# Kernel tuning notes

Hardware: AMD Instinct MI355X
Metric: run time of the kernel (lower is better)

The kernel has to match this reference:

```python
import jax, jax.numpy as jnp
import numpy as np

D = 1024   # dim_mid
H = 16     # heads
DK = D // H  # d_k = d_v = 64
S = 2048   # seq_len
B = 1      # batch (module's reshape logic assumes batch==1)
EPS = 1e-5


def setup_inputs() -> dict:
    key = jax.random.key(0)
    ks = jax.random.split(key, 10)
    s = 0.02
    return dict(
        Q=jax.random.normal(ks[0], (B, S, D), dtype=jnp.float32),
        K=jax.random.normal(ks[1], (B, S, D), dtype=jnp.float32),
        V=jax.random.normal(ks[2], (B, S, D), dtype=jnp.float32),
        attn_mask=jax.random.randint(ks[3], (1, S, S), 0, 2).astype(bool),
        wq=jax.random.normal(ks[4], (H * DK, D), dtype=jnp.float32) * s,
        bq=jnp.zeros((H * DK,), dtype=jnp.float32),
        wk=jax.random.normal(ks[5], (H * DK, D), dtype=jnp.float32) * s,
        bk=jnp.zeros((H * DK,), dtype=jnp.float32),
        wv=jax.random.normal(ks[6], (H * DK, D), dtype=jnp.float32) * s,
        bv=jnp.zeros((H * DK,), dtype=jnp.float32),
        wo=jax.random.normal(ks[7], (D, H * DK), dtype=jnp.float32) * s,
        bo=jnp.zeros((D,), dtype=jnp.float32),
        gamma=jnp.ones((D,), dtype=jnp.float32),
        beta=jnp.zeros((D,), dtype=jnp.float32),
    )


def reference(Q, K, V, attn_mask, wq, bq, wk, bk, wv, bv, wo, bo, gamma, beta):
    b, s = Q.shape[0], Q.shape[1]
    # projections -> (B, H, S, d_k)
    q = (Q @ wq.T + bq).reshape(b, s, H, DK).transpose(0, 2, 1, 3)
    k = (K @ wk.T + bk).reshape(b, s, H, DK).transpose(0, 2, 1, 3)
    v = (V @ wv.T + bv).reshape(b, s, H, DK).transpose(0, 2, 1, 3)
    scores = jnp.einsum('bhqd,bhkd->bhqk', q, k) / np.float32(np.sqrt(DK))
    scores = jnp.where(attn_mask[:, None, :, :], jnp.float32(-1e9), scores)
    attn = jax.nn.softmax(scores, axis=-1)
    ctx = jnp.einsum('bhqk,bhkd->bhqd', attn, v)  # (B, H, S, d_v)
    # torch: squeeze(0).transpose(0,1).view(seq_len, -1, H*d_v)  (valid for B==1)
    ctx2 = ctx[0].transpose(1, 0, 2).reshape(s, 1, H * DK)  # (S, 1, H*d_v)
    out = (ctx2 @ wo.T + bo).transpose(1, 0, 2) + Q  # (1, S, D) residual
    mu = out.mean(-1, keepdims=True)
    var = out.var(-1, keepdims=True)
    out = (out - mu) / jnp.sqrt(var + EPS) * gamma + beta
    return out, attn, ctx2
```

## Files before the change

### kernel.cpp

```cpp
#include <hip/hip_runtime.h>
#include <stdint.h>

#define S_LEN 2048
#define D_MID 1024
#define N_HEADS 16
#define D_HEAD 64

typedef __attribute__((ext_vector_type(4))) float f32x4;
typedef __attribute__((ext_vector_type(8))) short bf16x8;

__device__ __forceinline__ unsigned short f2bf(float x) {
  unsigned int u = __builtin_bit_cast(unsigned int, x);
  u += 0x7fffu + ((u >> 16) & 1u);
  return (unsigned short)(u >> 16);
}
__device__ __forceinline__ float bf2f(unsigned short h) {
  unsigned int u = ((unsigned int)h) << 16;
  return __builtin_bit_cast(float, u);
}
__device__ __forceinline__ unsigned int pack2(float x, float y) {
  return (unsigned int)f2bf(x) | ((unsigned int)f2bf(y) << 16);
}

#define MFMA16(a, b, c) __builtin_amdgcn_mfma_f32_16x16x32_bf16((a), (b), (c), 0, 0, 0)

struct ProjParams {
  const float* A[3];
  const float* W[3];
  const float* B[3];
  unsigned short* O[3];
};

__global__ __launch_bounds__(256) void gemm_proj(ProjParams P) {
  const int z = blockIdx.z;
  const float* __restrict__ A = P.A[z];
  const float* __restrict__ W = P.W[z];
  const float* __restrict__ bias = P.B[z];
  unsigned short* __restrict__ O = P.O[z];

  __shared__ __align__(16) unsigned short As[128][56];
  __shared__ __align__(16) unsigned short Bs[128][56];

  const int tid = threadIdx.x;
  const int lane = tid & 63, w = tid >> 6;
  const int wm = w >> 1, wn = w & 1;
  const int l15 = lane & 15, lhi = lane >> 4;
  const int m0 = blockIdx.y * 128, n0 = blockIdx.x * 128;
  const int sr = tid >> 1, sc = (tid & 1) * 16;

  f32x4 acc[4][4] = {};

  for (int k0 = 0; k0 < D_MID; k0 += 32) {
    __syncthreads();
    {
      const float* a = A + (size_t)(m0 + sr) * D_MID + k0 + sc;
      float4 a0 = ((const float4*)a)[0], a1 = ((const float4*)a)[1];
      float4 a2 = ((const float4*)a)[2], a3 = ((const float4*)a)[3];
      uint4 wa0, wa1;
      wa0.x = pack2(a0.x, a0.y); wa0.y = pack2(a0.z, a0.w);
      wa0.z = pack2(a1.x, a1.y); wa0.w = pack2(a1.z, a1.w);
      wa1.x = pack2(a2.x, a2.y); wa1.y = pack2(a2.z, a2.w);
      wa1.z = pack2(a3.x, a3.y); wa1.w = pack2(a3.z, a3.w);
      *(uint4*)&As[sr][sc] = wa0;
      *(uint4*)&As[sr][sc + 8] = wa1;

      const float* b = W + (size_t)(n0 + sr) * D_MID + k0 + sc;
      float4 b0 = ((const float4*)b)[0], b1 = ((const float4*)b)[1];
      float4 b2 = ((const float4*)b)[2], b3 = ((const float4*)b)[3];
      uint4 wb0, wb1;
      wb0.x = pack2(b0.x, b0.y); wb0.y = pack2(b0.z, b0.w);
      wb0.z = pack2(b1.x, b1.y); wb0.w = pack2(b1.z, b1.w);
      wb1.x = pack2(b2.x, b2.y); wb1.y = pack2(b2.z, b2.w);
      wb1.z = pack2(b3.x, b3.y); wb1.w = pack2(b3.z, b3.w);
      *(uint4*)&Bs[sr][sc] = wb0;
      *(uint4*)&Bs[sr][sc + 8] = wb1;
    }
    __syncthreads();

    bf16x8 af[4], bfr[4];
#pragma unroll
    for (int a = 0; a < 4; ++a)
      af[a] = *(const bf16x8*)&As[wm * 64 + a * 16 + l15][lhi * 8];
#pragma unroll
    for (int b = 0; b < 4; ++b)
      bfr[b] = *(const bf16x8*)&Bs[wn * 64 + b * 16 + l15][lhi * 8];
#pragma unroll
    for (int a = 0; a < 4; ++a)
#pragma unroll
      for (int b = 0; b < 4; ++b) acc[a][b] = MFMA16(af[a], bfr[b], acc[a][b]);
  }

#pragma unroll
  for (int a = 0; a < 4; ++a)
#pragma unroll
    for (int b = 0; b < 4; ++b) {
      const int col = n0 + wn * 64 + b * 16 + l15;
      const float bv = bias[col];
#pragma unroll
      for (int j = 0; j < 4; ++j) {
        const int row = m0 + wm * 64 + a * 16 + lhi * 4 + j;
        O[(size_t)row * D_MID + col] = f2bf(acc[a][b][j] + bv);
      }
    }
}

__global__ __launch_bounds__(256) void gemm_out(
    const float* __restrict__ Actx, const float* __restrict__ W,
    const float* __restrict__ bias, const float* __restrict__ resid,
    float* __restrict__ Of) {
  __shared__ __align__(16) unsigned short As[128][56];
  __shared__ __align__(16) unsigned short Bs[128][56];

  const int tid = threadIdx.x;
  const int lane = tid & 63, w = tid >> 6;
  const int wm = w >> 1, wn = w & 1;
  const int l15 = lane & 15, lhi = lane >> 4;
  const int m0 = blockIdx.y * 128, n0 = blockIdx.x * 128;
  const int sr = tid >> 1, sc = (tid & 1) * 16;

  f32x4 acc[4][4] = {};

  for (int k0 = 0; k0 < D_MID; k0 += 32) {
    __syncthreads();
    {
      const float* a = Actx + (size_t)(m0 + sr) * D_MID + k0 + sc;
      float4 a0 = ((const float4*)a)[0], a1 = ((const float4*)a)[1];
      float4 a2 = ((const float4*)a)[2], a3 = ((const float4*)a)[3];
      uint4 wa0, wa1;
      wa0.x = pack2(a0.x, a0.y); wa0.y = pack2(a0.z, a0.w);
      wa0.z = pack2(a1.x, a1.y); wa0.w = pack2(a1.z, a1.w);
      wa1.x = pack2(a2.x, a2.y); wa1.y = pack2(a2.z, a2.w);
      wa1.z = pack2(a3.x, a3.y); wa1.w = pack2(a3.z, a3.w);
      *(uint4*)&As[sr][sc] = wa0;
      *(uint4*)&As[sr][sc + 8] = wa1;

      const float* b = W + (size_t)(n0 + sr) * D_MID + k0 + sc;
      float4 b0 = ((const float4*)b)[0], b1 = ((const float4*)b)[1];
      float4 b2 = ((const float4*)b)[2], b3 = ((const float4*)b)[3];
      uint4 wb0, wb1;
      wb0.x = pack2(b0.x, b0.y); wb0.y = pack2(b0.z, b0.w);
      wb0.z = pack2(b1.x, b1.y); wb0.w = pack2(b1.z, b1.w);
      wb1.x = pack2(b2.x, b2.y); wb1.y = pack2(b2.z, b2.w);
      wb1.z = pack2(b3.x, b3.y); wb1.w = pack2(b3.z, b3.w);
      *(uint4*)&Bs[sr][sc] = wb0;
      *(uint4*)&Bs[sr][sc + 8] = wb1;
    }
    __syncthreads();

    bf16x8 af[4], bfr[4];
#pragma unroll
    for (int a = 0; a < 4; ++a)
      af[a] = *(const bf16x8*)&As[wm * 64 + a * 16 + l15][lhi * 8];
#pragma unroll
    for (int b = 0; b < 4; ++b)
      bfr[b] = *(const bf16x8*)&Bs[wn * 64 + b * 16 + l15][lhi * 8];
#pragma unroll
    for (int a = 0; a < 4; ++a)
#pragma unroll
      for (int b = 0; b < 4; ++b) acc[a][b] = MFMA16(af[a], bfr[b], acc[a][b]);
  }

#pragma unroll
  for (int a = 0; a < 4; ++a)
#pragma unroll
    for (int b = 0; b < 4; ++b) {
      const int col = n0 + wn * 64 + b * 16 + l15;
      const float bv = bias[col];
#pragma unroll
      for (int j = 0; j < 4; ++j) {
        const int row = m0 + wm * 64 + a * 16 + lhi * 4 + j;
        Of[(size_t)row * D_MID + col] =
            acc[a][b][j] + bv + resid[(size_t)row * D_MID + col];
      }
    }
}

__global__ __launch_bounds__(256) void transpose_to_vbt(
    const unsigned short* __restrict__ v, unsigned short* __restrict__ vt) {
  __shared__ __align__(16) unsigned short t[64][72];
  const int tid = threadIdx.x;
  const int bs = blockIdx.x * 64;
  const int bd = blockIdx.y * 64;
  {
    const int r = tid >> 2, c = (tid & 3) * 16;
    const unsigned short* src = v + (size_t)(bs + r) * D_MID + bd + c;
    *(uint4*)&t[r][c] = *(const uint4*)src;
    *(uint4*)&t[r][c + 8] = *(const uint4*)(src + 8);
  }
  __syncthreads();
  {
    const int d = tid >> 2, c = (tid & 3) * 16;
    unsigned int u[8];
#pragma unroll
    for (int jj = 0; jj < 8; ++jj)
      u[jj] = (unsigned int)t[c + 2 * jj][d] | ((unsigned int)t[c + 2 * jj + 1][d] << 16);
    uint4 w0, w1;
    w0.x = u[0]; w0.y = u[1]; w0.z = u[2]; w0.w = u[3];
    w1.x = u[4]; w1.y = u[5]; w1.z = u[6]; w1.w = u[7];
    unsigned short* dst = vt + (size_t)(bd + d) * S_LEN + bs + c;
    *(uint4*)dst = w0;
    *(uint4*)(dst + 8) = w1;
  }
}

__global__ __launch_bounds__(256) void pack_mask(const void* __restrict__ maskp,
                                                 unsigned long long* __restrict__ bits) {
  __shared__ int s_m32;
  if (threadIdx.x == 0) s_m32 = 1;
  __syncthreads();
  {
    const unsigned char* m8d = (const unsigned char*)maskp;
    bool nz = false;
    for (int i = threadIdx.x; i < 4096; i += 256)
      if (i & 3) nz |= (m8d[i] != 0);
    if (nz) s_m32 = 0;
  }
  __syncthreads();

  const int wi = blockIdx.x * 256 + threadIdx.x;
  const int row = wi >> 5, chunk = wi & 31;
  unsigned long long keep = 0ull;
  if (s_m32) {
    const int* mi = (const int*)maskp + (size_t)row * S_LEN + chunk * 64;
#pragma unroll
    for (int q = 0; q < 16; ++q) {
      int4 v = ((const int4*)mi)[q];
      const int b = q * 4;
      if (!v.x) keep |= 1ull << b;
      if (!v.y) keep |= 1ull << (b + 1);
      if (!v.z) keep |= 1ull << (b + 2);
      if (!v.w) keep |= 1ull << (b + 3);
    }
  } else {
    const unsigned char* p = (const unsigned char*)maskp + (size_t)row * S_LEN + chunk * 64;
    union { uint4 v[4]; unsigned char c[64]; } u;
#pragma unroll
    for (int q = 0; q < 4; ++q) u.v[q] = ((const uint4*)p)[q];
#pragma unroll
    for (int b = 0; b < 64; ++b)
      if (!u.c[b]) keep |= 1ull << b;
  }
  bits[wi] = keep;
}

__global__ __launch_bounds__(256) void lsum_kernel(
    const unsigned short* __restrict__ qb, const unsigned short* __restrict__ kb,
    const unsigned long long* __restrict__ bits, float* __restrict__ lpart) {
  const int bid = blockIdx.x;
  const int head = bid & 15;
  const int r = bid >> 4;
  const int q0 = (r & 31) * 64;
  const int kc = r >> 5;
  const int k0 = kc * (S_LEN / 4);

  const int tid = threadIdx.x;
  const int lane = tid & 63, w = tid >> 6;
  const int l15 = lane & 15, lhi = lane >> 4;

  __shared__ __align__(16) unsigned short Kt[64][72];

  bf16x8 aq[2];
  {
    const unsigned short* qp =
        qb + (size_t)(q0 + w * 16 + l15) * D_MID + head * D_HEAD + lhi * 8;
    aq[0] = *(const bf16x8*)qp;
    aq[1] = *(const bf16x8*)(qp + 32);
  }

  float lrow[4] = {0.f, 0.f, 0.f, 0.f};
  const int sk = tid >> 2, sc = (tid & 3) * 16;

  for (int kt = k0; kt < k0 + S_LEN / 4; kt += 64) {
    __syncthreads();
    {
      const unsigned short* src = kb + (size_t)(kt + sk) * D_MID + head * D_HEAD + sc;
      *(uint4*)&Kt[sk][sc] = *(const uint4*)src;
      *(uint4*)&Kt[sk][sc + 8] = *(const uint4*)(src + 8);
    }
    __syncthreads();

    f32x4 sacc[4];
#pragma unroll
    for (int a = 0; a < 4; ++a) {
      bf16x8 b0 = *(const bf16x8*)&Kt[a * 16 + l15][lhi * 8];
      bf16x8 b1 = *(const bf16x8*)&Kt[a * 16 + l15][32 + lhi * 8];
      f32x4 t = {0.f, 0.f, 0.f, 0.f};
      t = MFMA16(aq[0], b0, t);
      t = MFMA16(aq[1], b1, t);
      sacc[a] = t;
    }

#pragma unroll
    for (int j = 0; j < 4; ++j) {
      const int qg = q0 + w * 16 + lhi * 4 + j;
      const unsigned long long w64 = bits[(size_t)qg * 32 + (kt >> 6)];
      float ts = 0.f;
#pragma unroll
      for (int a = 0; a < 4; ++a) {
        const float keep = (float)((w64 >> (a * 16 + l15)) & 1ull);
        ts += __expf(sacc[a][j] * 0.125f) * keep;
      }
#pragma unroll
      for (int off = 1; off < 16; off <<= 1) ts += __shfl_xor(ts, off);
      lrow[j] += ts;
    }
  }

  if (l15 == 0) {
#pragma unroll
    for (int j = 0; j < 4; ++j) {
      const int qg = q0 + w * 16 + lhi * 4 + j;
      lpart[((size_t)kc * N_HEADS + head) * S_LEN + qg] = lrow[j];
    }
  }
}

__global__ __launch_bounds__(256) void lcombine(const float* __restrict__ lpart,
                                                float* __restrict__ linv) {
  const int i = blockIdx.x * 256 + threadIdx.x;
  const float s = lpart[i] + lpart[32768 + i] + lpart[65536 + i] + lpart[98304 + i];
  linv[i] = (s > 0.f) ? 1.f / s : 0.f;
}

__global__ __launch_bounds__(256) void attn_main(
    const unsigned short* __restrict__ qb, const unsigned short* __restrict__ kb,
    const unsigned short* __restrict__ vbt, const unsigned long long* __restrict__ bits,
    const float* __restrict__ linv, float* __restrict__ attn_out,
    unsigned short* __restrict__ ctxp, int nkc) {
  const int bid = blockIdx.x;
  const int head = bid & 15;
  const int r = bid >> 4;
  const int q0 = (r & 31) * 64;
  const int kc = r >> 5;
  const int kspan = S_LEN / nkc;
  const int k_begin = kc * kspan;

  const int tid = threadIdx.x;
  const int lane = tid & 63, w = tid >> 6;
  const int l15 = lane & 15, lhi = lane >> 4;

  __shared__ __align__(16) unsigned short Kt[64][72];
  __shared__ __align__(16) unsigned short Vt[64][72];
  __shared__ __align__(16) unsigned short Pl[4][16][76];

  bf16x8 aq[2];
  float li[4];
  {
    const int qrow = q0 + w * 16 + l15;
    const unsigned short* qp = qb + (size_t)qrow * D_MID + head * D_HEAD + lhi * 8;
    aq[0] = *(const bf16x8*)qp;
    aq[1] = *(const bf16x8*)(qp + 32);
#pragma unroll
    for (int j = 0; j < 4; ++j)
      li[j] = linv[head * S_LEN + q0 + w * 16 + lhi * 4 + j];
  }

  f32x4 cacc[4] = {};
  const int sk = tid >> 2, sc = (tid & 3) * 16;

  for (int kt = k_begin; kt < k_begin + kspan; kt += 64) {
    __syncthreads();
    {
      const unsigned short* srck = kb + (size_t)(kt + sk) * D_MID + head * D_HEAD + sc;
      *(uint4*)&Kt[sk][sc] = *(const uint4*)srck;
      *(uint4*)&Kt[sk][sc + 8] = *(const uint4*)(srck + 8);
      const unsigned short* srcv = vbt + (size_t)(head * D_HEAD + sk) * S_LEN + kt + sc;
      *(uint4*)&Vt[sk][sc] = *(const uint4*)srcv;
      *(uint4*)&Vt[sk][sc + 8] = *(const uint4*)(srcv + 8);
    }
    __syncthreads();

    f32x4 sacc[4];
#pragma unroll
    for (int a = 0; a < 4; ++a) {
      bf16x8 b0 = *(const bf16x8*)&Kt[a * 16 + l15][lhi * 8];
      bf16x8 b1 = *(const bf16x8*)&Kt[a * 16 + l15][32 + lhi * 8];
      f32x4 t = {0.f, 0.f, 0.f, 0.f};
      t = MFMA16(aq[0], b0, t);
      t = MFMA16(aq[1], b1, t);
      sacc[a] = t;
    }

#pragma unroll
    for (int j = 0; j < 4; ++j) {
      const int qg = q0 + w * 16 + lhi * 4 + j;
      const unsigned long long w64 = bits[(size_t)qg * 32 + (kt >> 6)];
      float* arow = attn_out + (size_t)head * S_LEN * S_LEN + (size_t)qg * S_LEN + kt;
#pragma unroll
      for (int a = 0; a < 4; ++a) {
        const float keep = (float)((w64 >> (a * 16 + l15)) & 1ull);
        const float p = __expf(sacc[a][j] * 0.125f) * keep * li[j];
        arow[a * 16 + l15] = p;
        Pl[w][lhi * 4 + j][a * 16 + l15] = f2bf(p);
      }
    }

    bf16x8 pa0 = *(const bf16x8*)&Pl[w][l15][lhi * 8];
    bf16x8 pa1 = *(const bf16x8*)&Pl[w][l15][32 + lhi * 8];
#pragma unroll
    for (int n = 0; n < 4; ++n) {
      bf16x8 v0 = *(const bf16x8*)&Vt[n * 16 + l15][lhi * 8];
      bf16x8 v1 = *(const bf16x8*)&Vt[n * 16 + l15][32 + lhi * 8];
      cacc[n] = MFMA16(pa0, v0, cacc[n]);
      cacc[n] = MFMA16(pa1, v1, cacc[n]);
    }
  }

  unsigned short* cp = ctxp + (size_t)kc * S_LEN * D_MID;
#pragma unroll
  for (int n = 0; n < 4; ++n)
#pragma unroll
    for (int j = 0; j < 4; ++j) {
      const int qg = q0 + w * 16 + lhi * 4 + j;
      const int col = head * D_HEAD + n * 16 + l15;
      cp[(size_t)qg * D_MID + col] = f2bf(cacc[n][j]);
    }
}

__global__ __launch_bounds__(256) void ctx_reduce(const unsigned short* __restrict__ ctxp,
                                                  float* __restrict__ ctx2, int nkc) {
  const int i = blockIdx.x * 256 + threadIdx.x;
  ushort4 a = ((const ushort4*)ctxp)[i];
  float4 o;
  o.x = bf2f(a.x); o.y = bf2f(a.y); o.z = bf2f(a.z); o.w = bf2f(a.w);
  if (nkc == 2) {
    ushort4 b = ((const ushort4*)(ctxp + (size_t)S_LEN * D_MID))[i];
    o.x += bf2f(b.x); o.y += bf2f(b.y); o.z += bf2f(b.z); o.w += bf2f(b.w);
  }
  ((float4*)ctx2)[i] = o;
}

__global__ __launch_bounds__(256) void layernorm_k(
    const float* __restrict__ x, const float* __restrict__ gamma,
    const float* __restrict__ beta, float* __restrict__ out) {
  const int row = blockIdx.x;
  const int tid = threadIdx.x;
  float4 v = ((const float4*)(x + (size_t)row * D_MID))[tid];
  float s = v.x + v.y + v.z + v.w;
  float s2 = v.x * v.x + v.y * v.y + v.z * v.z + v.w * v.w;
#pragma unroll
  for (int off = 1; off < 64; off <<= 1) {
    s += __shfl_xor(s, off);
    s2 += __shfl_xor(s2, off);
  }
  __shared__ float ps[4], ps2[4];
  const int w = tid >> 6;
  if ((tid & 63) == 0) { ps[w] = s; ps2[w] = s2; }
  __syncthreads();
  s = ps[0] + ps[1] + ps[2] + ps[3];
  s2 = ps2[0] + ps2[1] + ps2[2] + ps2[3];
  const float mu = s * (1.0f / D_MID);
  const float var = s2 * (1.0f / D_MID) - mu * mu;
  const float inv = rsqrtf(var + 1e-5f);
  float4 g = ((const float4*)gamma)[tid];
  float4 b = ((const float4*)beta)[tid];
  float4 o;
  o.x = (v.x - mu) * inv * g.x + b.x;
  o.y = (v.y - mu) * inv * g.y + b.y;
  o.z = (v.z - mu) * inv * g.z + b.z;
  o.w = (v.w - mu) * inv * g.w + b.w;
  ((float4*)(out + (size_t)row * D_MID))[tid] = o;
}

extern "C" void kernel_launch(void* const* d_in, const int* in_sizes, int n_in,
                              void* d_out, int out_size, void* d_ws, size_t ws_size,
                              hipStream_t stream) {
  (void)in_sizes; (void)n_in; (void)out_size;
  const float* Q = (const float*)d_in[0];
  const float* K = (const float*)d_in[1];
  const float* V = (const float*)d_in[2];
  const void* mask = d_in[3];
  const float* wq = (const float*)d_in[4];
  const float* bq = (const float*)d_in[5];
  const float* wk = (const float*)d_in[6];
  const float* bk = (const float*)d_in[7];
  const float* wv = (const float*)d_in[8];
  const float* bv = (const float*)d_in[9];
  const float* wo = (const float*)d_in[10];
  const float* bo = (const float*)d_in[11];
  const float* gamma = (const float*)d_in[12];
  const float* beta = (const float*)d_in[13];

  float* out = (float*)d_out;
  float* attn = out + (size_t)S_LEN * D_MID;
  float* ctx2 = attn + (size_t)N_HEADS * S_LEN * S_LEN;

  unsigned char* ws = (unsigned char*)d_ws;
  unsigned short* qb   = (unsigned short*)(ws);
  unsigned short* kbuf = (unsigned short*)(ws + (size_t)(4 << 20));
  unsigned short* vbuf = (unsigned short*)(ws + (size_t)(8 << 20));
  unsigned short* vbt  = (unsigned short*)(ws + (size_t)(12 << 20));
  unsigned long long* bits = (unsigned long long*)(ws + (size_t)(16 << 20));
  float* lpart = (float*)(ws + (size_t)(16 << 20) + 524288);
  float* linv  = (float*)(ws + (size_t)(17 << 20) + 262144);
  unsigned short* ctxp = (unsigned short*)(ws + (size_t)(18 << 20));
  float* preLN = (float*)(ws);

  const size_t need2 = (size_t)(18 << 20) + 2 * (size_t)S_LEN * D_MID * 2;
  const int nkc = (ws_size >= need2) ? 2 : 1;

  ProjParams pp;
  pp.A[0] = Q;  pp.W[0] = wq; pp.B[0] = bq; pp.O[0] = qb;
  pp.A[1] = K;  pp.W[1] = wk; pp.B[1] = bk; pp.O[1] = kbuf;
  pp.A[2] = V;  pp.W[2] = wv; pp.B[2] = bv; pp.O[2] = vbuf;

  gemm_proj<<<dim3(D_MID / 128, S_LEN / 128, 3), 256, 0, stream>>>(pp);
  pack_mask<<<256, 256, 0, stream>>>(mask, bits);
  transpose_to_vbt<<<dim3(S_LEN / 64, D_MID / 64), 256, 0, stream>>>(vbuf, vbt);
  lsum_kernel<<<2048, 256, 0, stream>>>(qb, kbuf, bits, lpart);
  lcombine<<<128, 256, 0, stream>>>(lpart, linv);
  attn_main<<<512 * nkc, 256, 0, stream>>>(qb, kbuf, vbt, bits, linv, attn, ctxp, nkc);
  ctx_reduce<<<(S_LEN * D_MID / 4) / 256, 256, 0, stream>>>(ctxp, ctx2, nkc);
  gemm_out<<<dim3(D_MID / 128, S_LEN / 128), 256, 0, stream>>>(ctx2, wo, bo, Q, preLN);
  layernorm_k<<<S_LEN, 256, 0, stream>>>(preLN, gamma, beta, out);
}
```

Baseline: 248.8 us.

## Register-prefetch K/V tiles and vectorize attention-probability stores via LDS

Both the row-sum and main attention kernels now load the next K (and V) tile into registers while computing on the current LDS tile, overlapping global latency with MFMA work. In the row-sum kernel the cross-lane shuffle reduction moves out of the tile loop and runs once at the end. In the main kernel, probabilities are staged in fp32 LDS and written to the large attention output with 16-byte nontemporal row-contiguous stores instead of scattered scalar stores. The bf16 MFMA operands are packed from that LDS buffer. The cost is more registers and more LDS for the fp32 staging buffer.

```diff
diff --git a/kernel.cpp b/kernel.cpp
--- a/kernel.cpp
+++ b/kernel.cpp
@@ -20,6 +20,12 @@
 }
 __device__ __forceinline__ unsigned int pack2(float x, float y) {
   return (unsigned int)f2bf(x) | ((unsigned int)f2bf(y) << 16);
+}
+__device__ __forceinline__ bf16x8 pack8(f32x4 a, f32x4 b) {
+  uint4 u;
+  u.x = pack2(a.x, a.y); u.y = pack2(a.z, a.w);
+  u.z = pack2(b.x, b.y); u.w = pack2(b.z, b.w);
+  return __builtin_bit_cast(bf16x8, u);
 }
 
 #define MFMA16(a, b, c) __builtin_amdgcn_mfma_f32_16x16x32_bf16((a), (b), (c), 0, 0, 0)
@@ -267,50 +273,65 @@
     aq[1] = *(const bf16x8*)(qp + 32);
   }
 
-  float lrow[4] = {0.f, 0.f, 0.f, 0.f};
+  float plrow[4] = {0.f, 0.f, 0.f, 0.f};
   const int sk = tid >> 2, sc = (tid & 3) * 16;
 
-  for (int kt = k0; kt < k0 + S_LEN / 4; kt += 64) {
-    __syncthreads();
-    {
-      const unsigned short* src = kb + (size_t)(kt + sk) * D_MID + head * D_HEAD + sc;
-      *(uint4*)&Kt[sk][sc] = *(const uint4*)src;
-      *(uint4*)&Kt[sk][sc + 8] = *(const uint4*)(src + 8);
-    }
-    __syncthreads();
+  const int ntiles = (S_LEN / 4) / 64;
+  uint4 kr0, kr1;
+  {
+    const unsigned short* src = kb + (size_t)(k0 + sk) * D_MID + head * D_HEAD + sc;
+    kr0 = *(const uint4*)src;
+    kr1 = *(const uint4*)(src + 8);
+  }
+
+  for (int t = 0; t < ntiles; ++t) {
+    const int kt = k0 + t * 64;
+    __syncthreads();
+    *(uint4*)&Kt[sk][sc] = kr0;
+    *(uint4*)&Kt[sk][sc + 8] = kr1;
+    __syncthreads();
+    if (t + 1 < ntiles) {
+      const unsigned short* src =
+          kb + (size_t)(kt + 64 + sk) * D_MID + head * D_HEAD + sc;
+      kr0 = *(const uint4*)src;
+      kr1 = *(const uint4*)(src + 8);
+    }
 
     f32x4 sacc[4];
 #pragma unroll
     for (int a = 0; a < 4; ++a) {
       bf16x8 b0 = *(const bf16x8*)&Kt[a * 16 + l15][lhi * 8];
       bf16x8 b1 = *(const bf16x8*)&Kt[a * 16 + l15][32 + lhi * 8];
-      f32x4 t = {0.f, 0.f, 0.f, 0.f};
-      t = MFMA16(aq[0], b0, t);
-      t = MFMA16(aq[1], b1, t);
-      sacc[a] = t;
+      f32x4 t2 = {0.f, 0.f, 0.f, 0.f};
+      t2 = MFMA16(aq[0], b0, t2);
+      t2 = MFMA16(aq[1], b1, t2);
+      sacc[a] = t2;
     }
 
 #pragma unroll
     for (int j = 0; j < 4; ++j) {
       const int qg = q0 + w * 16 + lhi * 4 + j;
       const unsigned long long w64 = bits[(size_t)qg * 32 + (kt >> 6)];
-      float ts = 0.f;
 #pragma unroll
       for (int a = 0; a < 4; ++a) {
         const float keep = (float)((w64 >> (a * 16 + l15)) & 1ull);
-        ts += __expf(sacc[a][j] * 0.125f) * keep;
+        plrow[j] += __expf(sacc[a][j] * 0.125f) * keep;
       }
-#pragma unroll
-      for (int off = 1; off < 16; off <<= 1) ts += __shfl_xor(ts, off);
-      lrow[j] += ts;
-    }
-  }
-
+    }
+  }
+
+#pragma unroll
+  for (int j = 0; j < 4; ++j) {
+    float ts = plrow[j];
+#pragma unroll
+    for (int off = 1; off < 16; off <<= 1) ts += __shfl_xor(ts, off);
+    plrow[j] = ts;
+  }
   if (l15 == 0) {
 #pragma unroll
     for (int j = 0; j < 4; ++j) {
       const int qg = q0 + w * 16 + lhi * 4 + j;
-      lpart[((size_t)kc * N_HEADS + head) * S_LEN + qg] = lrow[j];
+      lpart[((size_t)kc * N_HEADS + head) * S_LEN + qg] = plrow[j];
     }
   }
 }
@@ -341,7 +362,7 @@
 
   __shared__ __align__(16) unsigned short Kt[64][72];
   __shared__ __align__(16) unsigned short Vt[64][72];
-  __shared__ __align__(16) unsigned short Pl[4][16][76];
+  __shared__ __align__(16) float PF[4][16][68];
 
   bf16x8 aq[2];
   float li[4];
@@ -357,46 +378,73 @@
 
   f32x4 cacc[4] = {};
   const int sk = tid >> 2, sc = (tid & 3) * 16;
-
-  for (int kt = k_begin; kt < k_begin + kspan; kt += 64) {
-    __syncthreads();
-    {
-      const unsigned short* srck = kb + (size_t)(kt + sk) * D_MID + head * D_HEAD + sc;
-      *(uint4*)&Kt[sk][sc] = *(const uint4*)srck;
-      *(uint4*)&Kt[sk][sc + 8] = *(const uint4*)(srck + 8);
-      const unsigned short* srcv = vbt + (size_t)(head * D_HEAD + sk) * S_LEN + kt + sc;
-      *(uint4*)&Vt[sk][sc] = *(const uint4*)srcv;
-      *(uint4*)&Vt[sk][sc + 8] = *(const uint4*)(srcv + 8);
-    }
-    __syncthreads();
+  const int ntiles = kspan / 64;
+
+  uint4 kr0, kr1, vr0, vr1;
+  {
+    const unsigned short* srck = kb + (size_t)(k_begin + sk) * D_MID + head * D_HEAD + sc;
+    kr0 = *(const uint4*)srck;
+    kr1 = *(const uint4*)(srck + 8);
+    const unsigned short* srcv = vbt + (size_t)(head * D_HEAD + sk) * S_LEN + k_begin + sc;
+    vr0 = *(const uint4*)srcv;
+    vr1 = *(const uint4*)(srcv + 8);
+  }
+
+  for (int t = 0; t < ntiles; ++t) {
+    const int kt = k_begin + t * 64;
+    __syncthreads();
+    *(uint4*)&Kt[sk][sc] = kr0;
+    *(uint4*)&Kt[sk][sc + 8] = kr1;
+    *(uint4*)&Vt[sk][sc] = vr0;
+    *(uint4*)&Vt[sk][sc + 8] = vr1;
+    __syncthreads();
+    if (t + 1 < ntiles) {
+      const int kn = kt + 64;
+      const unsigned short* srck = kb + (size_t)(kn + sk) * D_MID + head * D_HEAD + sc;
+      kr0 = *(const uint4*)srck;
+      kr1 = *(const uint4*)(srck + 8);
+      const unsigned short* srcv = vbt + (size_t)(head * D_HEAD + sk) * S_LEN + kn + sc;
+      vr0 = *(const uint4*)srcv;
+      vr1 = *(const uint4*)(srcv + 8);
+    }
 
     f32x4 sacc[4];
 #pragma unroll
     for (int a = 0; a < 4; ++a) {
       bf16x8 b0 = *(const bf16x8*)&Kt[a * 16 + l15][lhi * 8];
       bf16x8 b1 = *(const bf16x8*)&Kt[a * 16 + l15][32 + lhi * 8];
-      f32x4 t = {0.f, 0.f, 0.f, 0.f};
-      t = MFMA16(aq[0], b0, t);
-      t = MFMA16(aq[1], b1, t);
-      sacc[a] = t;
+      f32x4 t2 = {0.f, 0.f, 0.f, 0.f};
+      t2 = MFMA16(aq[0], b0, t2);
+      t2 = MFMA16(aq[1], b1, t2);
+      sacc[a] = t2;
     }
 
 #pragma unroll
     for (int j = 0; j < 4; ++j) {
       const int qg = q0 + w * 16 + lhi * 4 + j;
       const unsigned long long w64 = bits[(size_t)qg * 32 + (kt >> 6)];
-      float* arow = attn_out + (size_t)head * S_LEN * S_LEN + (size_t)qg * S_LEN + kt;
 #pragma unroll
       for (int a = 0; a < 4; ++a) {
         const float keep = (float)((w64 >> (a * 16 + l15)) & 1ull);
-        const float p = __expf(sacc[a][j] * 0.125f) * keep * li[j];
-        arow[a * 16 + l15] = p;
-        Pl[w][lhi * 4 + j][a * 16 + l15] = f2bf(p);
+        PF[w][lhi * 4 + j][a * 16 + l15] = __expf(sacc[a][j] * 0.125f) * keep * li[j];
       }
     }
 
-    bf16x8 pa0 = *(const bf16x8*)&Pl[w][l15][lhi * 8];
-    bf16x8 pa1 = *(const bf16x8*)&Pl[w][l15][32 + lhi * 8];
+    {
+      float* abase = attn_out + (size_t)head * S_LEN * S_LEN +
+                     (size_t)(q0 + w * 16) * S_LEN + kt;
+#pragma unroll
+      for (int g = 0; g < 4; ++g) {
+        const int row = g * 4 + lhi;
+        f32x4 v = *(const f32x4*)&PF[w][row][l15 * 4];
+        __builtin_nontemporal_store(v, (f32x4*)(abase + (size_t)row * S_LEN + l15 * 4));
+      }
+    }
+
+    bf16x8 pa0 = pack8(*(const f32x4*)&PF[w][l15][lhi * 8],
+                       *(const f32x4*)&PF[w][l15][lhi * 8 + 4]);
+    bf16x8 pa1 = pack8(*(const f32x4*)&PF[w][l15][32 + lhi * 8],
+                       *(const f32x4*)&PF[w][l15][36 + lhi * 8]);
 #pragma unroll
     for (int n = 0; n < 4; ++n) {
       bf16x8 v0 = *(const bf16x8*)&Vt[n * 16 + l15][lhi * 8];
```

Measured after the change: 230.8 us. 1.08x faster.
